# Performance work log

Measured on AMD Instinct MI355X. Metric: run time of the kernel, lower is better.

## Reference

```python
import jax, jax.numpy as jnp
import numpy as np

B, S, D = 2, 2048, 2048
H, KV, HD, RD = 16, 4, 128, 64
EPS = 1e-6


def rotate_half(x):
    x1, x2 = jnp.split(x, 2, axis=-1)
    return jnp.concatenate([-x2, x1], axis=-1)


def rms_norm(x, w, eps=EPS):
    xf = x.astype(jnp.float32)
    r = jax.lax.rsqrt(jnp.mean(xf * xf, axis=-1, keepdims=True) + eps)
    return (w * xf * r).astype(x.dtype)


def setup_inputs() -> dict:
    key = jax.random.key(0)
    ks = jax.random.split(key, 8)
    x = jax.random.normal(ks[0], (B, S, D), dtype=jnp.float32)
    # real partial-RoPE angles
    pos = jnp.arange(S, dtype=jnp.float32)
    inv_freq = 1.0 / (10000.0 ** (jnp.arange(0, RD, 2, dtype=jnp.float32) / RD))
    ang = pos[:, None] * inv_freq[None, :]            # [S, RD/2]
    ang = jnp.concatenate([ang, ang], axis=-1)        # [S, RD]
    cos = jnp.broadcast_to(jnp.cos(ang), (B, S, RD))
    sin = jnp.broadcast_to(jnp.sin(ang), (B, S, RD))
    sc = 0.02
    wq = jax.random.normal(ks[1], (D, H * HD * 2), dtype=jnp.float32) * sc
    wk = jax.random.normal(ks[2], (D, KV * HD), dtype=jnp.float32) * sc
    wv = jax.random.normal(ks[3], (D, KV * HD), dtype=jnp.float32) * sc
    wo = jax.random.normal(ks[4], (H * HD, D), dtype=jnp.float32) * sc
    q_norm_w = jnp.ones((HD,), dtype=jnp.float32)
    k_norm_w = jnp.ones((HD,), dtype=jnp.float32)
    return {"x": x, "cos": cos, "sin": sin, "wq": wq, "wk": wk, "wv": wv,
            "wo": wo, "q_norm_w": q_norm_w, "k_norm_w": k_norm_w}


def reference(x, cos, sin, wq, wk, wv, wo, q_norm_w, k_norm_w):
    b, s, _ = x.shape
    n_rep = H // KV

    qg = (x @ wq).reshape(b, s, H, 2 * HD)
    query, gate = qg[..., :HD], qg[..., HD:]
    gate = gate.reshape(b, s, H * HD)

    query = rms_norm(query, q_norm_w)                              # [b,s,H,HD]
    key = rms_norm((x @ wk).reshape(b, s, KV, HD), k_norm_w)       # [b,s,KV,HD]
    value = (x @ wv).reshape(b, s, KV, HD)

    query = query.transpose(0, 2, 1, 3)   # [b,H,s,HD]
    key = key.transpose(0, 2, 1, 3)       # [b,KV,s,HD]
    value = value.transpose(0, 2, 1, 3)

    c = cos[:, None]  # [b,1,s,RD]
    si = sin[:, None]
    q_rot, q_pass = query[..., :RD], query[..., RD:]
    k_rot, k_pass = key[..., :RD], key[..., RD:]
    q_rot = q_rot * c + rotate_half(q_rot) * si
    k_rot = k_rot * c + rotate_half(k_rot) * si
    query = jnp.concatenate([q_rot, q_pass], axis=-1)
    key = jnp.concatenate([k_rot, k_pass], axis=-1)

    # GQA without materializing repeated K/V: group q heads by kv head
    qg_ = query.reshape(b, KV, n_rep, s, HD)
    scale = HD ** -0.5
    attn = jnp.einsum('bgrsd,bgtd->bgrst', qg_, key) * scale       # [b,KV,rep,s,s]
    causal = jnp.triu(jnp.full((s, s), -jnp.inf, dtype=attn.dtype), 1)
    attn = attn + causal
    attn = jax.nn.softmax(attn.astype(jnp.float32), axis=-1).astype(query.dtype)
    out = jnp.einsum('bgrst,bgtd->bgrsd', attn, value)             # [b,KV,rep,s,HD]
    out = out.reshape(b, H, s, HD).transpose(0, 2, 1, 3).reshape(b, s, H * HD)
    out = out * jax.nn.sigmoid(gate)
    return out @ wo, key, value
```

## Files before the change

kernel.cpp:

```cpp
#include <hip/hip_runtime.h>
#include <stdint.h>

typedef __attribute__((ext_vector_type(8))) __bf16 bf16x8;
typedef __attribute__((ext_vector_type(4))) float f32x4;

union frag_u { uint4 q; unsigned short s[8]; bf16x8 v; };

__device__ __forceinline__ float b2f(unsigned short u) {
    union { float f; unsigned int u; } x; x.u = ((unsigned int)u) << 16; return x.f;
}
__device__ __forceinline__ unsigned short f2b(float f) {
    union { float f; unsigned int u; } x; x.f = f;
    unsigned int r = x.u + 0x7fffu + ((x.u >> 16) & 1u);
    return (unsigned short)(r >> 16);
}

template<int AMODE, int BMODE, int CMODE, int KVF>
__global__ __launch_bounds__(256) void gemm_k(
    const void* __restrict__ Av, const void* __restrict__ Bv, const float* __restrict__ B2,
    void* __restrict__ Cv, void* __restrict__ C2v, int N, int K)
{
    __shared__ __align__(16) unsigned short Al[128 * 40];
    __shared__ __align__(16) unsigned short Bl[(BMODE == 1) ? 128 * 40 : 8];
    const void* Ap = Av;
    const float* Bp = (const float*)Bv;
    const unsigned short* Bt = (const unsigned short*)Bv;
    void* Cp = Cv;
    void* C2p = C2v;
    if (KVF == 1 && blockIdx.z) { Bp = B2; Cp = C2v; }
    if (KVF == 2 && blockIdx.z) {
        Ap  = (const float*)Av + 4194304;
        Cp  = (unsigned short*)Cv  + 8388608;
        C2p = (unsigned short*)C2v + 8388608;
    }
    const int tid = threadIdx.x;
    const int w = tid >> 6, l = tid & 63, quad = l >> 4, l16 = l & 15;
    const int wm = (w >> 1) * 64, wn = (w & 1) * 64;
    const int m0 = blockIdx.x * 128, n0 = blockIdx.y * 128;
    f32x4 acc[4][4] = {};
    for (int k0 = 0; k0 < K; k0 += 32) {
        __syncthreads();
#pragma unroll
        for (int i = 0; i < 2; ++i) {
            int chunk = tid + i * 256;
            int row = chunk >> 2, ko = (chunk & 3) * 8;
            if (AMODE == 0) {
                const float* src = (const float*)Ap + (size_t)(m0 + row) * K + k0 + ko;
                float4 f0 = *(const float4*)src;
                float4 f1 = *(const float4*)(src + 4);
                unsigned short t[8] = { f2b(f0.x), f2b(f0.y), f2b(f0.z), f2b(f0.w),
                                        f2b(f1.x), f2b(f1.y), f2b(f1.z), f2b(f1.w) };
                *(uint4*)(Al + row * 40 + ko) = *(const uint4*)t;
            } else {
                const unsigned short* src = (const unsigned short*)Ap + (size_t)(m0 + row) * K + k0 + ko;
                *(uint4*)(Al + row * 40 + ko) = *(const uint4*)src;
            }
            if (BMODE == 1) {
                const unsigned short* bsrc = Bt + (size_t)(n0 + row) * K + k0 + ko;
                *(uint4*)(Bl + row * 40 + ko) = *(const uint4*)bsrc;
            }
        }
        __syncthreads();
        frag_u af[4];
#pragma unroll
        for (int mt = 0; mt < 4; ++mt)
            af[mt].q = *(const uint4*)(Al + (wm + mt * 16 + l16) * 40 + quad * 8);
#pragma unroll
        for (int nt = 0; nt < 4; ++nt) {
            frag_u bf_;
            if (BMODE == 1) {
                bf_.q = *(const uint4*)(Bl + (wn + nt * 16 + l16) * 40 + quad * 8);
            } else {
                const float* bp = Bp + (size_t)(k0 + quad * 8) * N + (n0 + wn + nt * 16 + l16);
#pragma unroll
                for (int j = 0; j < 8; ++j) bf_.s[j] = f2b(bp[(size_t)j * N]);
            }
#pragma unroll
            for (int mt = 0; mt < 4; ++mt)
                acc[mt][nt] = __builtin_amdgcn_mfma_f32_16x16x32_bf16(af[mt].v, bf_.v, acc[mt][nt], 0, 0, 0);
        }
    }
#pragma unroll
    for (int mt = 0; mt < 4; ++mt)
#pragma unroll
        for (int nt = 0; nt < 4; ++nt)
#pragma unroll
            for (int r = 0; r < 4; ++r) {
                int row = m0 + wm + mt * 16 + quad * 4 + r;
                int col = n0 + wn + nt * 16 + l16;
                float vacc = acc[mt][nt][r];
                if (CMODE == 0) {
                    ((float*)Cp)[(size_t)row * N + col] = vacc;
                } else if (CMODE == 1) {
                    ((float*)Cp)[(size_t)((row >> 11) * 4 + (col >> 7)) * 262144
                                 + (size_t)(row & 2047) * 128 + (col & 127)] = vacc;
                } else {
                    int hh = col >> 8, dd = col & 255;
                    unsigned short v = f2b(vacc);
                    if (dd < 128) ((unsigned short*)Cp )[(size_t)row * 2048 + hh * 128 + dd]         = v;
                    else          ((unsigned short*)C2p)[(size_t)row * 2048 + hh * 128 + (dd - 128)] = v;
                }
            }
}

__global__ __launch_bounds__(256) void wtrans(
    const float* __restrict__ W, unsigned short* __restrict__ Wt, int N, int K)
{
    __shared__ unsigned short T[128 * 65];
    const int tid = threadIdx.x;
    const int k0 = blockIdx.x * 64;
    const int n0 = blockIdx.y * 128;
    const float* src = W + (size_t)k0 * N + n0;
#pragma unroll
    for (int i = 0; i < 8; ++i) {
        int idx = tid + i * 256;
        int row = idx >> 5, c4 = (idx & 31) * 4;
        float4 f = *(const float4*)(src + (size_t)row * N + c4);
        T[(c4 + 0) * 65 + row] = f2b(f.x);
        T[(c4 + 1) * 65 + row] = f2b(f.y);
        T[(c4 + 2) * 65 + row] = f2b(f.z);
        T[(c4 + 3) * 65 + row] = f2b(f.w);
    }
    __syncthreads();
#pragma unroll
    for (int i = 0; i < 4; ++i) {
        int idx = tid + i * 256;
        int d = idx >> 3, sc = (idx & 7) * 8;
        unsigned short o8[8];
#pragma unroll
        for (int j = 0; j < 8; ++j) o8[j] = T[d * 65 + sc + j];
        *(uint4*)(Wt + (size_t)(n0 + d) * K + k0 + sc) = *(const uint4*)o8;
    }
}

__global__ __launch_bounds__(256) void knorm_rope(
    float* __restrict__ Kp, unsigned short* __restrict__ Kb16,
    const float* __restrict__ nw,
    const float* __restrict__ cosb, const float* __restrict__ sinb)
{
    const int tid = threadIdx.x, w = tid >> 6, l = tid & 63;
    const int s = blockIdx.x * 4 + w, kv = blockIdx.y, b = blockIdx.z;
    float* row = Kp + (size_t)((b * 4 + kv) * 2048 + s) * 128;
    float x0 = row[l], x1 = row[l + 64];
    float ss = x0 * x0 + x1 * x1;
#pragma unroll
    for (int m = 1; m < 64; m <<= 1) ss += __shfl_xor(ss, m, 64);
    float r = rsqrtf(ss * (1.0f / 128.0f) + 1e-6f);
    float y0 = x0 * r * nw[l];
    float y1 = x1 * r * nw[l + 64];
    float p = __shfl_xor(y0, 32, 64);
    float c  = cosb[(size_t)(b * 2048 + s) * 64 + l];
    float si = sinb[(size_t)(b * 2048 + s) * 64 + l];
    float yr = y0 * c + (l < 32 ? -p : p) * si;
    row[l] = yr;
    row[l + 64] = y1;
    unsigned short* kb = Kb16 + (size_t)((b * 4 + kv) * 2048 + s) * 128;
    kb[l]      = f2b(yr);
    kb[l + 64] = f2b(y1);
}

__global__ __launch_bounds__(256) void vconv(
    const float* __restrict__ V, unsigned short* __restrict__ Vt)
{
    __shared__ unsigned short T[128 * 65];
    const int tid = threadIdx.x;
    const int s0 = blockIdx.x * 64;
    const int bk = blockIdx.y;
    const float* src = V + (size_t)bk * 262144 + (size_t)s0 * 128;
#pragma unroll
    for (int i = 0; i < 8; ++i) {
        int idx = tid + i * 256;
        int row = idx >> 5, c4 = (idx & 31) * 4;
        float4 f = *(const float4*)(src + (size_t)row * 128 + c4);
        T[(c4 + 0) * 65 + row] = f2b(f.x);
        T[(c4 + 1) * 65 + row] = f2b(f.y);
        T[(c4 + 2) * 65 + row] = f2b(f.z);
        T[(c4 + 3) * 65 + row] = f2b(f.w);
    }
    __syncthreads();
    unsigned short* dst = Vt + (size_t)bk * 262144 + s0;
#pragma unroll
    for (int i = 0; i < 4; ++i) {
        int idx = tid + i * 256;
        int d = idx >> 3, sc = (idx & 7) * 8;
        unsigned short o8[8];
#pragma unroll
        for (int j = 0; j < 8; ++j) o8[j] = T[d * 65 + sc + j];
        *(uint4*)(dst + (size_t)d * 2048 + sc) = *(const uint4*)o8;
    }
}

__global__ __launch_bounds__(256) void attn(
    const unsigned short* __restrict__ Qall, const unsigned short* __restrict__ K16,
    const unsigned short* __restrict__ V16, unsigned short* __restrict__ Oall,
    const float* __restrict__ cosall, const float* __restrict__ sinall,
    const float* __restrict__ qnw)
{
    __shared__ __align__(16) unsigned short KVl[32 * 136 + 128 * 40];
    __shared__ __align__(16) unsigned short Pb[4][16 * 40];
    __shared__ __align__(16) float Ab[4][16];
    unsigned short* Kl = KVl;
    unsigned short* Vl = KVl + 32 * 136;
    const int tid = threadIdx.x, w = tid >> 6, l = tid & 63, quad = l >> 4, l16 = l & 15;
    const int bb = blockIdx.z;
    const int gx = blockIdx.x;
    const int h = blockIdx.y, kv = h >> 2;
    const unsigned short* Qb = Qall + (size_t)bb * 8388608;
    const unsigned short* Gb = Qb + 4194304;
    unsigned short* Ob = Oall + (size_t)bb * 4194304;
    const float* cosb_ = cosall + (size_t)bb * 131072;
    const float* sinb_ = sinall + (size_t)bb * 131072;
    const unsigned short* Kb = K16 + (size_t)(bb * 4 + kv) * 262144;
    const unsigned short* Vb = V16 + (size_t)(bb * 4 + kv) * 262144;
    const float SCALE = 0.08838834764831845f;
    const float NEG = -30000.0f;

    for (int pp = 0; pp < 2; ++pp) {
        const int g = pp ? (31 - gx) : gx;
        const int qt = g * 4 + w;
        const int srow = qt * 16 + l16;
        const unsigned short* qrow = Qb + (size_t)srow * 2048 + h * 128;
        frag_u qraw[4];
#pragma unroll
        for (int kk = 0; kk < 4; ++kk) qraw[kk].q = *(const uint4*)(qrow + kk * 32 + quad * 8);
        float qv[4][8];
        float ss = 0.f;
#pragma unroll
        for (int kk = 0; kk < 4; ++kk)
#pragma unroll
            for (int j = 0; j < 8; ++j) { qv[kk][j] = b2f(qraw[kk].s[j]); ss += qv[kk][j] * qv[kk][j]; }
        ss += __shfl_xor(ss, 16, 64);
        ss += __shfl_xor(ss, 32, 64);
        const float rn = rsqrtf(ss * (1.0f / 128.0f) + 1e-6f);
#pragma unroll
        for (int kk = 0; kk < 4; ++kk)
#pragma unroll
            for (int j = 0; j < 8; ++j) qv[kk][j] *= rn * qnw[kk * 32 + quad * 8 + j];
        const float* csrow = cosb_ + (size_t)srow * 64;
        const float* sirow = sinb_ + (size_t)srow * 64;
#pragma unroll
        for (int j = 0; j < 8; ++j) {
            float a0 = qv[0][j], a1 = qv[1][j];
            float c0 = csrow[quad * 8 + j],      s0 = sirow[quad * 8 + j];
            float c1 = csrow[32 + quad * 8 + j], s1 = sirow[32 + quad * 8 + j];
            qv[0][j] = a0 * c0 - a1 * s0;
            qv[1][j] = a1 * c1 + a0 * s1;
        }
        frag_u qf[4];
#pragma unroll
        for (int kk = 0; kk < 4; ++kk)
#pragma unroll
            for (int j = 0; j < 8; ++j) qf[kk].s[j] = f2b(qv[kk][j]);

        f32x4 O[8] = {};
        float M[4], Lp[4];
#pragma unroll
        for (int r = 0; r < 4; ++r) { M[r] = NEG; Lp[r] = 0.f; }
        const int qr_base = qt * 16 + quad * 4;
        const int T_blk = 2 * g + 2;
        const int T_w = 2 * g + 1 + (w >> 1);

        for (int kt = 0; kt < T_blk; ++kt) {
            const int kbase = kt * 32;
            __syncthreads();
#pragma unroll
            for (int i = 0; i < 2; ++i) {
                int s = tid + i * 256;
                int kr = s >> 4, kseg = s & 15;
                *(uint4*)(Kl + kr * 136 + kseg * 8) =
                    *(const uint4*)(Kb + (size_t)(kbase + kr) * 128 + kseg * 8);
                int d = s >> 2, vseg = s & 3;
                *(uint4*)(Vl + d * 40 + vseg * 8) =
                    *(const uint4*)(Vb + (size_t)d * 2048 + kbase + vseg * 8);
            }
            __syncthreads();
            if (kt >= T_w) continue;
            f32x4 sc0 = {}, sc1 = {};
#pragma unroll
            for (int kk = 0; kk < 4; ++kk) {
                frag_u kf0, kf1;
                kf0.q = *(const uint4*)(Kl + (l16)      * 136 + kk * 32 + quad * 8);
                kf1.q = *(const uint4*)(Kl + (16 + l16) * 136 + kk * 32 + quad * 8);
                sc0 = __builtin_amdgcn_mfma_f32_16x16x32_bf16(qf[kk].v, kf0.v, sc0, 0, 0, 0);
                sc1 = __builtin_amdgcn_mfma_f32_16x16x32_bf16(qf[kk].v, kf1.v, sc1, 0, 0, 0);
            }
            float s0a[4], s1a[4], p0[4], p1[4], tm[4];
            const bool lastt = (kt == T_w - 1);
            bool ok = true;
#pragma unroll
            for (int r = 0; r < 4; ++r) {
                float s0 = sc0[r] * SCALE, s1 = sc1[r] * SCALE;
                if (lastt) {
                    if (kbase + l16 > qr_base + r)      s0 = NEG;
                    if (kbase + 16 + l16 > qr_base + r) s1 = NEG;
                }
                s0a[r] = s0; s1a[r] = s1;
                p0[r] = __expf(s0 - M[r]);
                p1[r] = __expf(s1 - M[r]);
                float m = fmaxf(s0, s1);
                m = fmaxf(m, __shfl_xor(m, 1, 64));
                m = fmaxf(m, __shfl_xor(m, 2, 64));
                m = fmaxf(m, __shfl_xor(m, 4, 64));
                m = fmaxf(m, __shfl_xor(m, 8, 64));
                tm[r] = m;
                ok = ok && (m <= M[r] + 8.0f);
            }
            if (!__all(ok)) {
#pragma unroll
                for (int r = 0; r < 4; ++r) {
                    float mn = fmaxf(M[r], tm[r]);
                    float alpha = __expf(M[r] - mn);
                    p0[r] = __expf(s0a[r] - mn);
                    p1[r] = __expf(s1a[r] - mn);
                    Lp[r] *= alpha;
                    M[r] = mn;
                    if (l16 == 0) Ab[w][quad * 4 + r] = alpha;
                }
                float ao = Ab[w][l16];
#pragma unroll
                for (int dt = 0; dt < 8; ++dt) {
                    O[dt][0] *= ao; O[dt][1] *= ao; O[dt][2] *= ao; O[dt][3] *= ao;
                }
            }
#pragma unroll
            for (int r = 0; r < 4; ++r) {
                Lp[r] += p0[r] + p1[r];
                Pb[w][(quad * 4 + r) * 40 + l16]      = f2b(p0[r]);
                Pb[w][(quad * 4 + r) * 40 + 16 + l16] = f2b(p1[r]);
            }
            frag_u pf;
            pf.q = *(const uint4*)(Pb[w] + l16 * 40 + quad * 8);
#pragma unroll
            for (int dt = 0; dt < 8; ++dt) {
                frag_u vf;
                vf.q = *(const uint4*)(Vl + (dt * 16 + l16) * 40 + quad * 8);
                O[dt] = __builtin_amdgcn_mfma_f32_16x16x32_bf16(vf.v, pf.v, O[dt], 0, 0, 0);
            }
        }
        __syncthreads();
        unsigned short* Ol = KVl + w * 2176;
#pragma unroll
        for (int r = 0; r < 4; ++r) {
            float ls = Lp[r];
            ls += __shfl_xor(ls, 1, 64);
            ls += __shfl_xor(ls, 2, 64);
            ls += __shfl_xor(ls, 4, 64);
            ls += __shfl_xor(ls, 8, 64);
            if (l16 == 0) Ab[w][quad * 4 + r] = ls;
        }
        float rl = 1.0f / Ab[w][l16];
#pragma unroll
        for (int dt = 0; dt < 8; ++dt) {
            unsigned int u0 = (unsigned int)f2b(O[dt][0] * rl) | ((unsigned int)f2b(O[dt][1] * rl) << 16);
            unsigned int u1 = (unsigned int)f2b(O[dt][2] * rl) | ((unsigned int)f2b(O[dt][3] * rl) << 16);
            uint2 u; u.x = u0; u.y = u1;
            *(uint2*)(Ol + l16 * 136 + dt * 16 + quad * 4) = u;
        }
#pragma unroll
        for (int i = 0; i < 4; ++i) {
            int c2 = l + i * 64;
            int row = c2 >> 4, off = (c2 & 15) * 8;
            uint4 v = *(const uint4*)(Ol + row * 136 + off);
            const unsigned short* vs = (const unsigned short*)&v;
            size_t rb = (size_t)(qt * 16 + row) * 2048 + h * 128 + off;
            uint4 g4 = *(const uint4*)(Gb + rb);
            const unsigned short* gs = (const unsigned short*)&g4;
            unsigned short o8[8];
#pragma unroll
            for (int j = 0; j < 8; ++j) {
                float o = b2f(vs[j]), gg = b2f(gs[j]);
                o8[j] = f2b(o / (1.0f + __expf(-gg)));
            }
            *(uint4*)(Ob + rb) = *(const uint4*)o8;
        }
    }
}

extern "C" void kernel_launch(void* const* d_in, const int* in_sizes, int n_in,
                              void* d_out, int out_size, void* d_ws, size_t ws_size,
                              hipStream_t stream)
{
    const float* x    = (const float*)d_in[0];
    const float* cosb = (const float*)d_in[1];
    const float* sinb = (const float*)d_in[2];
    const float* wq   = (const float*)d_in[3];
    const float* wk   = (const float*)d_in[4];
    const float* wv   = (const float*)d_in[5];
    const float* wo   = (const float*)d_in[6];
    const float* qnw  = (const float*)d_in[7];
    const float* knw  = (const float*)d_in[8];

    float* out = (float*)d_out;
    float* KEY = out + 8388608;
    float* VAL = out + 10485760;

    unsigned short* outs = (unsigned short*)d_out;
    unsigned short* xg   = (unsigned short*)d_in[0];
    unsigned short* K16  = xg + 8388608;
    unsigned short* V16  = xg + 10485760;
    unsigned short* wqT  = (unsigned short*)KEY;
    unsigned short* woT  = xg + 12582912;

    wtrans<<<dim3(32, 32), 256, 0, stream>>>(wq, wqT, 4096, 2048);

    gemm_k<0,1,2,2><<<dim3(16, 32, 2), 256, 0, stream>>>(x, wqT, nullptr,
                                                         outs, outs + 4194304, 4096, 2048);

    gemm_k<0,0,1,1><<<dim3(32, 4, 2), 256, 0, stream>>>(x, wk, wv, KEY, VAL, 512, 2048);

    knorm_rope<<<dim3(512, 4, 2), 256, 0, stream>>>(KEY, K16, knw, cosb, sinb);
    vconv<<<dim3(32, 8), 256, 0, stream>>>(VAL, V16);

    wtrans<<<dim3(32, 16), 256, 0, stream>>>(wo, woT, 2048, 2048);

    attn<<<dim3(16, 16, 2), 256, 0, stream>>>(outs, K16, V16, xg, cosb, sinb, qnw);

    gemm_k<1,1,0,0><<<dim3(32, 16), 256, 0, stream>>>(xg, woT, nullptr, out, nullptr, 2048, 2048);
}
```

Before: 551.0 us.

## Pre-convert x and K/V weights to bf16 once and reuse in projection GEMMs

Adds an xconv kernel that converts x to bf16 a single time and transposes wk/wv to bf16. The Q and K/V projection GEMMs then read bf16 operands (AMODE/BMODE 1) instead of converting fp32 inside every tile load. This removes repeated fp32 loads and conversions across the many column blocks. In exchange it adds extra kernel launches and moves the scratch buffers between the output and input regions, which has to be handled carefully (attn now writes O over its own Q buffer).

```diff
diff --git a/kernel.cpp b/kernel.cpp
--- a/kernel.cpp
+++ b/kernel.cpp
@@ -27,11 +27,11 @@
     const unsigned short* Bt = (const unsigned short*)Bv;
     void* Cp = Cv;
     void* C2p = C2v;
-    if (KVF == 1 && blockIdx.z) { Bp = B2; Cp = C2v; }
+    if (KVF == 1 && blockIdx.z) { Bt = (const unsigned short*)B2; Cp = C2v; }
     if (KVF == 2 && blockIdx.z) {
-        Ap  = (const float*)Av + 4194304;
-        Cp  = (unsigned short*)Cv  + 8388608;
-        C2p = (unsigned short*)C2v + 8388608;
+        Ap  = (const unsigned short*)Av + 4194304;
+        Cp  = (unsigned short*)Cv  + 4194304;
+        C2p = (unsigned short*)C2v + 4194304;
     }
     const int tid = threadIdx.x;
     const int w = tid >> 6, l = tid & 63, quad = l >> 4, l16 = l & 15;
@@ -103,6 +103,17 @@
             }
 }
 
+__global__ __launch_bounds__(256) void xconv(
+    const float* __restrict__ X, unsigned short* __restrict__ X16)
+{
+    size_t i = ((size_t)blockIdx.x * 256 + threadIdx.x) * 8;
+    float4 f0 = *(const float4*)(X + i);
+    float4 f1 = *(const float4*)(X + i + 4);
+    unsigned short t[8] = { f2b(f0.x), f2b(f0.y), f2b(f0.z), f2b(f0.w),
+                            f2b(f1.x), f2b(f1.y), f2b(f1.z), f2b(f1.w) };
+    *(uint4*)(X16 + i) = *(const uint4*)t;
+}
+
 __global__ __launch_bounds__(256) void wtrans(
     const float* __restrict__ W, unsigned short* __restrict__ Wt, int N, int K)
 {
@@ -205,8 +216,8 @@
     const int bb = blockIdx.z;
     const int gx = blockIdx.x;
     const int h = blockIdx.y, kv = h >> 2;
-    const unsigned short* Qb = Qall + (size_t)bb * 8388608;
-    const unsigned short* Gb = Qb + 4194304;
+    const unsigned short* Qb = Qall + (size_t)bb * 4194304;
+    const unsigned short* Gb = Qall + 8388608 + (size_t)bb * 4194304;
     unsigned short* Ob = Oall + (size_t)bb * 4194304;
     const float* cosb_ = cosall + (size_t)bb * 131072;
     const float* sinb_ = sinall + (size_t)bb * 131072;
@@ -396,24 +407,31 @@
 
     unsigned short* outs = (unsigned short*)d_out;
     unsigned short* xg   = (unsigned short*)d_in[0];
-    unsigned short* K16  = xg + 8388608;
-    unsigned short* V16  = xg + 10485760;
-    unsigned short* wqT  = (unsigned short*)KEY;
-    unsigned short* woT  = xg + 12582912;
+    unsigned short* x16  = outs;
+    unsigned short* wqT  = outs + 8388608;
+    unsigned short* K16  = outs + 8388608;
+    unsigned short* V16  = outs + 10485760;
+    unsigned short* wkT  = xg;
+    unsigned short* wvT  = xg + 1048576;
+    unsigned short* woT  = xg + 8388608;
+
+    xconv<<<dim3(4096), 256, 0, stream>>>(x, x16);
 
     wtrans<<<dim3(32, 32), 256, 0, stream>>>(wq, wqT, 4096, 2048);
-
-    gemm_k<0,1,2,2><<<dim3(16, 32, 2), 256, 0, stream>>>(x, wqT, nullptr,
-                                                         outs, outs + 4194304, 4096, 2048);
-
-    gemm_k<0,0,1,1><<<dim3(32, 4, 2), 256, 0, stream>>>(x, wk, wv, KEY, VAL, 512, 2048);
+    wtrans<<<dim3(32, 4), 256, 0, stream>>>(wk, wkT, 512, 2048);
+    wtrans<<<dim3(32, 4), 256, 0, stream>>>(wv, wvT, 512, 2048);
+
+    gemm_k<1,1,1,1><<<dim3(32, 4, 2), 256, 0, stream>>>(x16, wkT, (const float*)wvT,
+                                                        KEY, VAL, 512, 2048);
+
+    gemm_k<1,1,2,2><<<dim3(16, 32, 2), 256, 0, stream>>>(x16, wqT, nullptr,
+                                                         xg, xg + 8388608, 4096, 2048);
 
     knorm_rope<<<dim3(512, 4, 2), 256, 0, stream>>>(KEY, K16, knw, cosb, sinb);
     vconv<<<dim3(32, 8), 256, 0, stream>>>(VAL, V16);
 
+    attn<<<dim3(16, 16, 2), 256, 0, stream>>>(xg, K16, V16, xg, cosb, sinb, qnw);
+
     wtrans<<<dim3(32, 16), 256, 0, stream>>>(wo, woT, 2048, 2048);
-
-    attn<<<dim3(16, 16, 2), 256, 0, stream>>>(outs, K16, V16, xg, cosb, sinb, qnw);
-
     gemm_k<1,1,0,0><<<dim3(32, 16), 256, 0, stream>>>(xg, woT, nullptr, out, nullptr, 2048, 2048);
 }
```

Result: faster. 497.1 us (-9.8%).
